# Optimization experiments

Measured on AMD Instinct MI355X. Metric: run time of the kernel, lower is better.

## Reference

```python
import jax, jax.numpy as jnp
import numpy as np

EPS = 1e-8  # matches TMLoss(eps=1e-08)


def setup_inputs() -> dict:
    key = jax.random.key(0)
    k1, k2 = jax.random.split(key)
    b, n = 2048, 1024
    # pseudo protein coords: spread out like real structures (~tens of Angstroms)
    pred = jax.random.normal(k1, (b, n, 3), dtype=jnp.float32) * 10.0
    # native coords = pred + noise, arbitrarily rotated/translated is fine since we Kabsch-align
    actual = pred + jax.random.normal(k2, (b, n, 3), dtype=jnp.float32)
    return {"predicted_coords": pred, "actual_coords": actual}


def _kabsch_align(align_to, align_from):
    """Rigidly align align_from onto align_to (batched Kabsch). Shapes (b,n,3)."""
    mu_to = jnp.mean(align_to, axis=1, keepdims=True)
    mu_from = jnp.mean(align_from, axis=1, keepdims=True)
    p = align_to - mu_to      # (b,n,3) target, centered
    q = align_from - mu_from  # (b,n,3) mobile, centered
    # 3x3 cross-covariance M = q^T p; optimal R maximizes tr(R^T M)
    M = jnp.einsum('bni,bnj->bij', q, p)  # (b,3,3)
    U, S, Vt = jnp.linalg.svd(M)
    # proper-rotation (det=+1) correction on smallest singular direction
    d = jnp.sign(jnp.linalg.det(U) * jnp.linalg.det(Vt))  # (b,)
    ones = jnp.ones_like(d)
    D = jnp.stack([ones, ones, d], axis=-1)               # (b,3)
    R = jnp.einsum('bik,bk,bkj->bij', U, D, Vt)           # (b,3,3)
    aligned = jnp.einsum('bni,bij->bnj', q, R) + mu_to    # (b,n,3)
    return align_to, aligned


def _calc_tm(dev, reduce=True):
    """dev: (b,n) per-residue deviations -> TM-score."""
    n = dev.shape[-1]
    d0 = 1.24 * (n - 15.0) ** (1.0 / 3.0) - 1.8
    tm = jnp.mean(1.0 / (1.0 + (dev / d0) ** 2), axis=-1)  # (b,)
    return jnp.mean(tm) if reduce else tm


def reference(predicted_coords, actual_coords):
    # align=True path: Kabsch-align native onto prediction
    _, aligned_actual = _kabsch_align(predicted_coords, actual_coords)
    # per-residue deviation (eps added elementwise before norm, as in torch source)
    dev = jnp.linalg.norm(predicted_coords - aligned_actual + EPS, axis=-1)  # (b,n)
    return -_calc_tm(dev, reduce=True)
```

## Files before the change

kernel.cpp:

```cpp
#include <hip/hip_runtime.h>
#include <math.h>

#define NRES 1024
#define TM_EPS 1e-8f

__global__ void tm_reduce1(const float* __restrict__ pred, const float* __restrict__ act,
                           float* __restrict__ sums) {
    int b = blockIdx.x;
    const float4* p4 = (const float4*)(pred + (size_t)b * NRES * 3);
    const float4* a4 = (const float4*)(act  + (size_t)b * NRES * 3);
    int t = threadIdx.x;

    float4 pf0 = p4[3 * t + 0], pf1 = p4[3 * t + 1], pf2 = p4[3 * t + 2];
    float4 af0 = a4[3 * t + 0], af1 = a4[3 * t + 1], af2 = a4[3 * t + 2];

    float px[4] = {pf0.x, pf0.w, pf1.z, pf2.y};
    float py[4] = {pf0.y, pf1.x, pf1.w, pf2.z};
    float pz[4] = {pf0.z, pf1.y, pf2.x, pf2.w};
    float ax[4] = {af0.x, af0.w, af1.z, af2.y};
    float ay[4] = {af0.y, af1.x, af1.w, af2.z};
    float az[4] = {af0.z, af1.y, af2.x, af2.w};

    float acc[15];
#pragma unroll
    for (int i = 0; i < 15; i++) acc[i] = 0.f;
#pragma unroll
    for (int r = 0; r < 4; r++) {
        acc[0] += px[r]; acc[1] += py[r]; acc[2] += pz[r];
        acc[3] += ax[r]; acc[4] += ay[r]; acc[5] += az[r];
        acc[6]  += ax[r] * px[r]; acc[7]  += ax[r] * py[r]; acc[8]  += ax[r] * pz[r];
        acc[9]  += ay[r] * px[r]; acc[10] += ay[r] * py[r]; acc[11] += ay[r] * pz[r];
        acc[12] += az[r] * px[r]; acc[13] += az[r] * py[r]; acc[14] += az[r] * pz[r];
    }

#pragma unroll
    for (int off = 32; off > 0; off >>= 1) {
#pragma unroll
        for (int i = 0; i < 15; i++) acc[i] += __shfl_down(acc[i], off);
    }
    __shared__ float red[4][15];
    int wave = threadIdx.x >> 6, lane = threadIdx.x & 63;
    if (lane == 0) {
#pragma unroll
        for (int i = 0; i < 15; i++) red[wave][i] = acc[i];
    }
    __syncthreads();
    if (threadIdx.x < 15) {
        int i = threadIdx.x;
        sums[(size_t)b * 16 + i] = red[0][i] + red[1][i] + red[2][i] + red[3][i];
    }
}

__global__ void tm_kabsch(const float* __restrict__ sums, float* __restrict__ rot, int B) {
    int b = blockIdx.x * blockDim.x + threadIdx.x;
    if (b >= B) return;
    const float* s = sums + (size_t)b * 16;
    const double n = (double)NRES;
    double mp[3], mq[3];
#pragma unroll
    for (int i = 0; i < 3; i++) { mp[i] = (double)s[i] / n; mq[i] = (double)s[3 + i] / n; }
    double M[3][3];
#pragma unroll
    for (int i = 0; i < 3; i++)
#pragma unroll
        for (int j = 0; j < 3; j++)
            M[i][j] = (double)s[6 + i * 3 + j] - n * mq[i] * mp[j];

    double Sxx = M[0][0], Sxy = M[0][1], Sxz = M[0][2];
    double Syx = M[1][0], Syy = M[1][1], Syz = M[1][2];
    double Szx = M[2][0], Szy = M[2][1], Szz = M[2][2];
    double a[4][4];
    a[0][0] = Sxx + Syy + Szz; a[0][1] = Syz - Szy;        a[0][2] = Szx - Sxz;         a[0][3] = Sxy - Syx;
    a[1][0] = a[0][1];         a[1][1] = Sxx - Syy - Szz;  a[1][2] = Sxy + Syx;         a[1][3] = Szx + Sxz;
    a[2][0] = a[0][2];         a[2][1] = a[1][2];          a[2][2] = -Sxx + Syy - Szz;  a[2][3] = Syz + Szy;
    a[3][0] = a[0][3];         a[3][1] = a[1][3];          a[3][2] = a[2][3];           a[3][3] = -Sxx - Syy + Szz;

    double v[4][4];
#pragma unroll
    for (int i = 0; i < 4; i++)
#pragma unroll
        for (int j = 0; j < 4; j++) v[i][j] = (i == j) ? 1.0 : 0.0;

    double fro = 0.0;
    for (int i = 0; i < 4; i++) for (int j = 0; j < 4; j++) fro += a[i][j] * a[i][j];
    fro = sqrt(fro) + 1e-300;

    for (int sweep = 0; sweep < 25; sweep++) {
        double off = 0.0;
        for (int p = 0; p < 3; p++) for (int q = p + 1; q < 4; q++) off += a[p][q] * a[p][q];
        if (off < 1e-26 * fro * fro) break;
        for (int p = 0; p < 3; p++) {
            for (int q = p + 1; q < 4; q++) {
                double apq = a[p][q];
                if (fabs(apq) < 1e-30 * fro) continue;
                double theta = (a[q][q] - a[p][p]) / (2.0 * apq);
                double tt = (theta >= 0.0 ? 1.0 : -1.0) / (fabs(theta) + sqrt(theta * theta + 1.0));
                double c = 1.0 / sqrt(tt * tt + 1.0), sv = tt * c;
                for (int k = 0; k < 4; k++) {
                    double akp = a[k][p], akq = a[k][q];
                    a[k][p] = c * akp - sv * akq;
                    a[k][q] = sv * akp + c * akq;
                }
                for (int k = 0; k < 4; k++) {
                    double apk = a[p][k], aqk = a[q][k];
                    a[p][k] = c * apk - sv * aqk;
                    a[q][k] = sv * apk + c * aqk;
                }
                for (int k = 0; k < 4; k++) {
                    double vkp = v[k][p], vkq = v[k][q];
                    v[k][p] = c * vkp - sv * vkq;
                    v[k][q] = sv * vkp + c * vkq;
                }
            }
        }
    }

    int best = 0;
    double bestval = a[0][0];
    for (int i = 1; i < 4; i++) if (a[i][i] > bestval) { bestval = a[i][i]; best = i; }
    double w = v[0][best], x = v[1][best], y = v[2][best], z = v[3][best];
    double nrm = sqrt(w * w + x * x + y * y + z * z);
    w /= nrm; x /= nrm; y /= nrm; z /= nrm;

    double A[3][3];
    A[0][0] = 1.0 - 2.0 * (y * y + z * z); A[0][1] = 2.0 * (x * y - w * z);       A[0][2] = 2.0 * (x * z + w * y);
    A[1][0] = 2.0 * (x * y + w * z);       A[1][1] = 1.0 - 2.0 * (x * x + z * z); A[1][2] = 2.0 * (y * z - w * x);
    A[2][0] = 2.0 * (x * z - w * y);       A[2][1] = 2.0 * (y * z + w * x);       A[2][2] = 1.0 - 2.0 * (x * x + y * y);

    float* o = rot + (size_t)b * 12;
#pragma unroll
    for (int i = 0; i < 3; i++)
#pragma unroll
        for (int j = 0; j < 3; j++) o[i * 3 + j] = (float)A[i][j];
#pragma unroll
    for (int i = 0; i < 3; i++)
        o[9 + i] = (float)(mp[i] - (A[i][0] * mq[0] + A[i][1] * mq[1] + A[i][2] * mq[2]));
}

__global__ void tm_score(const float* __restrict__ pred, const float* __restrict__ act,
                         const float* __restrict__ rot, float* __restrict__ out,
                         float scale, float inv_d02) {
    int b = blockIdx.x;
    const float* R = rot + (size_t)b * 12;
    float A00 = R[0], A01 = R[1], A02 = R[2];
    float A10 = R[3], A11 = R[4], A12 = R[5];
    float A20 = R[6], A21 = R[7], A22 = R[8];
    float t0 = R[9], t1 = R[10], t2 = R[11];

    const float4* p4 = (const float4*)(pred + (size_t)b * NRES * 3);
    const float4* a4 = (const float4*)(act  + (size_t)b * NRES * 3);
    int t = threadIdx.x;
    float4 pf0 = p4[3 * t + 0], pf1 = p4[3 * t + 1], pf2 = p4[3 * t + 2];
    float4 af0 = a4[3 * t + 0], af1 = a4[3 * t + 1], af2 = a4[3 * t + 2];

    float px[4] = {pf0.x, pf0.w, pf1.z, pf2.y};
    float py[4] = {pf0.y, pf1.x, pf1.w, pf2.z};
    float pz[4] = {pf0.z, pf1.y, pf2.x, pf2.w};
    float ax[4] = {af0.x, af0.w, af1.z, af2.y};
    float ay[4] = {af0.y, af1.x, af1.w, af2.z};
    float az[4] = {af0.z, af1.y, af2.x, af2.w};

    float s = 0.f;
#pragma unroll
    for (int r = 0; r < 4; r++) {
        float dx = px[r] - (A00 * ax[r] + A01 * ay[r] + A02 * az[r]) - t0 + TM_EPS;
        float dy = py[r] - (A10 * ax[r] + A11 * ay[r] + A12 * az[r]) - t1 + TM_EPS;
        float dz = pz[r] - (A20 * ax[r] + A21 * ay[r] + A22 * az[r]) - t2 + TM_EPS;
        float d2 = dx * dx + dy * dy + dz * dz;
        s += 1.0f / (1.0f + d2 * inv_d02);
    }
#pragma unroll
    for (int off = 32; off > 0; off >>= 1) s += __shfl_down(s, off);

    __shared__ float red[4];
    int wave = threadIdx.x >> 6, lane = threadIdx.x & 63;
    if (lane == 0) red[wave] = s;
    __syncthreads();
    if (threadIdx.x == 0) {
        float tot = red[0] + red[1] + red[2] + red[3];
        atomicAdd(out, -tot * scale);
    }
}

extern "C" void kernel_launch(void* const* d_in, const int* in_sizes, int n_in,
                              void* d_out, int out_size, void* d_ws, size_t ws_size,
                              hipStream_t stream) {
    const float* pred = (const float*)d_in[0];
    const float* act  = (const float*)d_in[1];
    float* out = (float*)d_out;
    int B = in_sizes[0] / (NRES * 3);

    float* ws   = (float*)d_ws;
    float* sums = ws;
    float* rot  = ws + (size_t)B * 16;

    hipMemsetAsync(d_out, 0, sizeof(float), stream);

    tm_reduce1<<<B, 256, 0, stream>>>(pred, act, sums);
    tm_kabsch<<<(B + 255) / 256, 256, 0, stream>>>(sums, rot, B);

    double d0 = 1.24 * cbrt((double)NRES - 15.0) - 1.8;
    float inv_d02 = (float)(1.0 / (d0 * d0));
    float scale = 1.0f / ((float)B * (float)NRES);
    tm_score<<<B, 256, 0, stream>>>(pred, act, rot, out, scale, inv_d02);
}
```

Before: 126.2 us.

## Replace Jacobi eigen-solve with Newton root of quaternion characteristic polynomial

Replaces the iterative double-precision Jacobi diagonalisation of the 4x4 quaternion key matrix with a closed-form approach. It builds the characteristic polynomial from traces of K, K^2 and K^4, runs a fixed 20-step Newton iteration from sqrt(p2) to find the largest eigenvalue, and takes the eigenvector as the row of the adjugate of K - λI with the largest norm. This removes the data-dependent sweep loops and branches in the per-batch kabsch kernel. The trade-off is possible precision loss for near-degenerate eigenvalues. The kabsch kernel is a small fraction of total time next to the two memory-bound passes.

```diff
diff --git a/kernel.cpp b/kernel.cpp
--- a/kernel.cpp
+++ b/kernel.cpp
@@ -69,56 +69,79 @@
     double Sxx = M[0][0], Sxy = M[0][1], Sxz = M[0][2];
     double Syx = M[1][0], Syy = M[1][1], Syz = M[1][2];
     double Szx = M[2][0], Szy = M[2][1], Szz = M[2][2];
-    double a[4][4];
-    a[0][0] = Sxx + Syy + Szz; a[0][1] = Syz - Szy;        a[0][2] = Szx - Sxz;         a[0][3] = Sxy - Syx;
-    a[1][0] = a[0][1];         a[1][1] = Sxx - Syy - Szz;  a[1][2] = Sxy + Syx;         a[1][3] = Szx + Sxz;
-    a[2][0] = a[0][2];         a[2][1] = a[1][2];          a[2][2] = -Sxx + Syy - Szz;  a[2][3] = Syz + Szy;
-    a[3][0] = a[0][3];         a[3][1] = a[1][3];          a[3][2] = a[2][3];           a[3][3] = -Sxx - Syy + Szz;
-
-    double v[4][4];
+    double K[4][4];
+    K[0][0] = Sxx + Syy + Szz; K[0][1] = Syz - Szy;        K[0][2] = Szx - Sxz;         K[0][3] = Sxy - Syx;
+    K[1][0] = K[0][1];         K[1][1] = Sxx - Syy - Szz;  K[1][2] = Sxy + Syx;         K[1][3] = Szx + Sxz;
+    K[2][0] = K[0][2];         K[2][1] = K[1][2];          K[2][2] = -Sxx + Syy - Szz;  K[2][3] = Syz + Szy;
+    K[3][0] = K[0][3];         K[3][1] = K[1][3];          K[3][2] = K[2][3];           K[3][3] = -Sxx - Syy + Szz;
+
+    double K2[4][4];
 #pragma unroll
     for (int i = 0; i < 4; i++)
 #pragma unroll
-        for (int j = 0; j < 4; j++) v[i][j] = (i == j) ? 1.0 : 0.0;
-
-    double fro = 0.0;
-    for (int i = 0; i < 4; i++) for (int j = 0; j < 4; j++) fro += a[i][j] * a[i][j];
-    fro = sqrt(fro) + 1e-300;
-
-    for (int sweep = 0; sweep < 25; sweep++) {
-        double off = 0.0;
-        for (int p = 0; p < 3; p++) for (int q = p + 1; q < 4; q++) off += a[p][q] * a[p][q];
-        if (off < 1e-26 * fro * fro) break;
-        for (int p = 0; p < 3; p++) {
-            for (int q = p + 1; q < 4; q++) {
-                double apq = a[p][q];
-                if (fabs(apq) < 1e-30 * fro) continue;
-                double theta = (a[q][q] - a[p][p]) / (2.0 * apq);
-                double tt = (theta >= 0.0 ? 1.0 : -1.0) / (fabs(theta) + sqrt(theta * theta + 1.0));
-                double c = 1.0 / sqrt(tt * tt + 1.0), sv = tt * c;
-                for (int k = 0; k < 4; k++) {
-                    double akp = a[k][p], akq = a[k][q];
-                    a[k][p] = c * akp - sv * akq;
-                    a[k][q] = sv * akp + c * akq;
-                }
-                for (int k = 0; k < 4; k++) {
-                    double apk = a[p][k], aqk = a[q][k];
-                    a[p][k] = c * apk - sv * aqk;
-                    a[q][k] = sv * apk + c * aqk;
-                }
-                for (int k = 0; k < 4; k++) {
-                    double vkp = v[k][p], vkq = v[k][q];
-                    v[k][p] = c * vkp - sv * vkq;
-                    v[k][q] = sv * vkp + c * vkq;
-                }
-            }
+        for (int j = 0; j < 4; j++) {
+            double acc = 0.0;
+#pragma unroll
+            for (int k = 0; k < 4; k++) acc += K[i][k] * K[k][j];
+            K2[i][j] = acc;
         }
-    }
-
-    int best = 0;
-    double bestval = a[0][0];
-    for (int i = 1; i < 4; i++) if (a[i][i] > bestval) { bestval = a[i][i]; best = i; }
-    double w = v[0][best], x = v[1][best], y = v[2][best], z = v[3][best];
+    double p2 = 0.0, p3 = 0.0, p4 = 0.0;
+#pragma unroll
+    for (int i = 0; i < 4; i++)
+#pragma unroll
+        for (int j = 0; j < 4; j++) {
+            p2 += K[i][j] * K[i][j];
+            p3 += K2[i][j] * K[i][j];
+            p4 += K2[i][j] * K2[i][j];
+        }
+    double e2 = -0.5 * p2;
+    double e3 = p3 / 3.0;
+    double e4 = (0.5 * p2 * p2 - p4) * 0.25;
+
+    double lam = sqrt(p2);
+#pragma unroll
+    for (int it = 0; it < 20; it++) {
+        double lam2 = lam * lam;
+        double P  = lam2 * lam2 + e2 * lam2 - e3 * lam + e4;
+        double Pp = 4.0 * lam * lam2 + 2.0 * e2 * lam - e3;
+        lam -= P / Pp;
+    }
+
+    double Bm[4][4];
+#pragma unroll
+    for (int i = 0; i < 4; i++)
+#pragma unroll
+        for (int j = 0; j < 4; j++) Bm[i][j] = K[i][j] - ((i == j) ? lam : 0.0);
+
+    double cand[4][4];
+#pragma unroll
+    for (int r = 0; r < 4; r++) {
+        int rr[3];
+        int k = 0;
+#pragma unroll
+        for (int i = 0; i < 4; i++) if (i != r) rr[k++] = i;
+#pragma unroll
+        for (int c = 0; c < 4; c++) {
+            int cc[3];
+            int m = 0;
+#pragma unroll
+            for (int j = 0; j < 4; j++) if (j != c) cc[m++] = j;
+            double d =
+                Bm[rr[0]][cc[0]] * (Bm[rr[1]][cc[1]] * Bm[rr[2]][cc[2]] - Bm[rr[1]][cc[2]] * Bm[rr[2]][cc[1]])
+              - Bm[rr[0]][cc[1]] * (Bm[rr[1]][cc[0]] * Bm[rr[2]][cc[2]] - Bm[rr[1]][cc[2]] * Bm[rr[2]][cc[0]])
+              + Bm[rr[0]][cc[2]] * (Bm[rr[1]][cc[0]] * Bm[rr[2]][cc[1]] - Bm[rr[1]][cc[1]] * Bm[rr[2]][cc[0]]);
+            cand[r][c] = (((r + c) & 1) ? -d : d);
+        }
+    }
+    int bestr = 0;
+    double bestn = -1.0;
+#pragma unroll
+    for (int r = 0; r < 4; r++) {
+        double nn = cand[r][0] * cand[r][0] + cand[r][1] * cand[r][1] +
+                    cand[r][2] * cand[r][2] + cand[r][3] * cand[r][3];
+        if (nn > bestn) { bestn = nn; bestr = r; }
+    }
+    double w = cand[bestr][0], x = cand[bestr][1], y = cand[bestr][2], z = cand[bestr][3];
     double nrm = sqrt(w * w + x * x + y * y + z * z);
     w /= nrm; x /= nrm; y /= nrm; z /= nrm;
 
```

Measured after the change: 120.3 us. -4.7%, faster.
